# Kernel tuning notes

Hardware: AMD Instinct MI355X
Metric: run time of the kernel (lower is better)

## Reference

```python
import jax, jax.numpy as jnp
import numpy as np
from jax import lax

# dims: S=seq_len, B=batch, D=word dim, HE=encoder hidden, HD=decoder hidden,
# E=atomic embedding dim, A=num_atomic, T=max_steps, SOS=start token id
S, B, D = 48, 64, 300
HE, HD, E, A, T, SOS = 300, 256, 50, 128, 50, 1


def _u(key, shape, scale):
    return jax.random.uniform(key, shape, jnp.float32, -scale, scale)


def setup_inputs() -> dict:
    key = jax.random.key(0)
    ks = iter(jax.random.split(key, 64))
    inp = {"word_vectors": jax.random.normal(next(ks), (S, B, D), jnp.float32)}
    se = 1.0 / np.sqrt(HE)
    for l, din in ((0, D), (1, 2 * HE)):
        for d in ("f", "b"):
            inp[f"e{l}{d}_Wih"] = _u(next(ks), (3 * HE, din), se)
            inp[f"e{l}{d}_Whh"] = _u(next(ks), (3 * HE, HE), se)
            inp[f"e{l}{d}_bih"] = _u(next(ks), (3 * HE,), se)
            inp[f"e{l}{d}_bhh"] = _u(next(ks), (3 * HE,), se)
    sd = 1.0 / np.sqrt(HD)
    for l, din in ((0, E), (1, HD)):
        inp[f"d{l}_Wih"] = _u(next(ks), (3 * HD, din), sd)
        inp[f"d{l}_Whh"] = _u(next(ks), (3 * HD, HD), sd)
        inp[f"d{l}_bih"] = _u(next(ks), (3 * HD,), sd)
        inp[f"d{l}_bhh"] = _u(next(ks), (3 * HD,), sd)
    emb = jax.random.normal(next(ks), (A, E), jnp.float32)
    inp["emb"] = emb.at[0].set(0.0)  # padding_idx=0
    inp["Wout"] = _u(next(ks), (A, HD), sd)
    inp["bout"] = _u(next(ks), (A,), sd)
    so = 1.0 / np.sqrt(D)
    inp["Wh0"] = _u(next(ks), (2 * HD, D), so)
    inp["bh0"] = _u(next(ks), (2 * HD,), so)
    return inp


def gru_cell(x, h, Wih, Whh, bih, bhh):
    # PyTorch GRU cell semantics
    gi = x @ Wih.T + bih
    gh = h @ Whh.T + bhh
    ir, iz, inn = jnp.split(gi, 3, axis=-1)
    hr, hz, hn = jnp.split(gh, 3, axis=-1)
    r = jax.nn.sigmoid(ir + hr)
    z = jax.nn.sigmoid(iz + hz)
    n = jnp.tanh(inn + r * hn)
    return (1.0 - z) * n + z * h


def gru_layer(xs, Wih, Whh, bih, bhh, reverse=False):
    # xs: [S, B, din] -> [S, B, H]; h0 = zeros (torch default)
    h0 = jnp.zeros((xs.shape[1], Whh.shape[1]), xs.dtype)
    def step(h, x):
        hn = gru_cell(x, h, Wih, Whh, bih, bhh)
        return hn, hn
    _, ys = lax.scan(step, h0, xs, reverse=reverse)
    return ys


def reference(word_vectors, e0f_Wih, e0f_Whh, e0f_bih, e0f_bhh, e0b_Wih, e0b_Whh, e0b_bih, e0b_bhh, e1f_Wih, e1f_Whh, e1f_bih, e1f_bhh, e1b_Wih, e1b_Whh, e1b_bih, e1b_bhh, d0_Wih, d0_Whh, d0_bih, d0_bhh, d1_Wih, d1_Whh, d1_bih, d1_bhh, emb, Wout, bout, Wh0, bh0):
    # --- encoder: 2-layer bidirectional GRU (eval mode: no dropout) ---
    x0f = gru_layer(word_vectors, e0f_Wih, e0f_Whh, e0f_bih, e0f_bhh, reverse=False)
    x0b = gru_layer(word_vectors, e0b_Wih, e0b_Whh, e0b_bih, e0b_bhh, reverse=True)
    x0 = jnp.concatenate([x0f, x0b], axis=-1)  # [S,B,2*HE]
    x1f = gru_layer(x0, e1f_Wih, e1f_Whh, e1f_bih, e1f_bhh, reverse=False)
    x1b = gru_layer(x0, e1b_Wih, e1b_Whh, e1b_bih, e1b_bhh, reverse=True)
    enc = x1f + x1b  # view(S,B,2,HE).sum(dim=2) of concat == sum of directions

    N = S * B
    h = jnp.tanh(enc @ Wh0.T + bh0).reshape(N, 2, HD)  # [N,2,HD]
    h0, h1 = h[:, 0], h[:, 1]
    e = jnp.broadcast_to(emb[SOS], (N, E))

    def step(carry, _):
        h0, h1, e = carry
        h0n = gru_cell(e, h0, d0_Wih, d0_Whh, d0_bih, d0_bhh)
        h1n = gru_cell(h0n, h1, d1_Wih, d1_Whh, d1_bih, d1_bhh)
        y = jax.nn.log_softmax(h1n @ Wout.T + bout, axis=-1)  # [N,A]
        p = jnp.argmax(y, axis=-1)
        return (h0n, h1n, emb[p]), y

    _, Y = lax.scan(step, (h0, h1, e), None, length=T)  # [T,N,A]
    return Y.reshape(T, S, B, A)[:-1]
```

## Files before the change

### kernel.cpp

```cpp
#include <hip/hip_runtime.h>
#include <math.h>

#define S_ 48
#define B_ 64
#define D_ 300
#define HE_ 300
#define HD_ 256
#define E_ 50
#define A_ 128
#define T_ 50
#define N_ (S_*B_)
#define NR 6

__device__ __forceinline__ float sigm(float x){ return 1.0f/(1.0f + expf(-x)); }

template<int MODE>
__global__ __launch_bounds__(256)
void gemm_bias_kernel(const float* __restrict__ A, const float* __restrict__ W,
                      const float* __restrict__ bias, float* __restrict__ C,
                      float* __restrict__ C2, int M, int N, int K)
{
  __shared__ float As[16][64];
  __shared__ float Ws[16][64];
  const int tid = threadIdx.x;
  const int bm = blockIdx.y * 64;
  const int bn = blockIdx.x * 64;
  const int tx = tid & 15, ty = tid >> 4;
  const int lr = tid >> 2;
  const int lk = (tid & 3) << 2;
  float acc[4][4] = {{0.f}};
  for (int kb = 0; kb < K; kb += 16) {
    {
      const int row = bm + lr;
      const int k = kb + lk;
      const float* ap = A + (size_t)row * K + k;
      float4 v = make_float4(0.f,0.f,0.f,0.f);
      if (k + 3 < K) v = *reinterpret_cast<const float4*>(ap);
      else {
        if (k   < K) v.x = ap[0];
        if (k+1 < K) v.y = ap[1];
        if (k+2 < K) v.z = ap[2];
        if (k+3 < K) v.w = ap[3];
      }
      As[lk][lr]=v.x; As[lk+1][lr]=v.y; As[lk+2][lr]=v.z; As[lk+3][lr]=v.w;
    }
    {
      const int col = bn + lr;
      const int k = kb + lk;
      float4 v = make_float4(0.f,0.f,0.f,0.f);
      if (col < N) {
        const float* wp = W + (size_t)col * K + k;
        if (k + 3 < K) v = *reinterpret_cast<const float4*>(wp);
        else {
          if (k   < K) v.x = wp[0];
          if (k+1 < K) v.y = wp[1];
          if (k+2 < K) v.z = wp[2];
          if (k+3 < K) v.w = wp[3];
        }
      }
      Ws[lk][lr]=v.x; Ws[lk+1][lr]=v.y; Ws[lk+2][lr]=v.z; Ws[lk+3][lr]=v.w;
    }
    __syncthreads();
    #pragma unroll
    for (int kk = 0; kk < 16; ++kk) {
      float4 a4 = *reinterpret_cast<const float4*>(&As[kk][ty<<2]);
      float4 w4 = *reinterpret_cast<const float4*>(&Ws[kk][tx<<2]);
      const float* a = reinterpret_cast<const float*>(&a4);
      const float* w = reinterpret_cast<const float*>(&w4);
      #pragma unroll
      for (int i = 0; i < 4; ++i)
        #pragma unroll
        for (int j = 0; j < 4; ++j)
          acc[i][j] = fmaf(a[i], w[j], acc[i][j]);
    }
    __syncthreads();
  }
  #pragma unroll
  for (int i = 0; i < 4; ++i) {
    const int m = bm + (ty<<2) + i;
    #pragma unroll
    for (int j = 0; j < 4; ++j) {
      const int n = bn + (tx<<2) + j;
      if (n < N) {
        float v = acc[i][j] + bias[n];
        if (MODE == 0) {
          C[(size_t)m*N + n] = v;
        } else {
          v = tanhf(v);
          if (n < HD_) C[(size_t)m*HD_ + n] = v;
          else         C2[(size_t)m*HD_ + (n-HD_)] = v;
        }
      }
    }
  }
}

__device__ __forceinline__ void tile_mac(const float (*As)[64], const float (*Ws)[16][36],
                                         int tcol, int trow,
                                         float* accr, float* accz, float* accn)
{
  #pragma unroll
  for (int kk = 0; kk < 32; kk += 4) {
    float4 wr4 = *reinterpret_cast<const float4*>(&Ws[0][tcol][kk]);
    float4 wz4 = *reinterpret_cast<const float4*>(&Ws[1][tcol][kk]);
    float4 wn4 = *reinterpret_cast<const float4*>(&Ws[2][tcol][kk]);
    const float* wr = reinterpret_cast<const float*>(&wr4);
    const float* wz = reinterpret_cast<const float*>(&wz4);
    const float* wn = reinterpret_cast<const float*>(&wn4);
    #pragma unroll
    for (int u = 0; u < 4; ++u) {
      float4 a4 = *reinterpret_cast<const float4*>(&As[kk+u][trow]);
      const float* a = reinterpret_cast<const float*>(&a4);
      #pragma unroll
      for (int q = 0; q < 4; ++q) {
        accr[q] = fmaf(a[q], wr[u], accr[q]);
        accz[q] = fmaf(a[q], wz[u], accz[q]);
        accn[q] = fmaf(a[q], wn[u], accn[q]);
      }
    }
  }
}

__global__ __launch_bounds__(256)
void enc_step_kernel(const float* __restrict__ gi_f, const float* __restrict__ gi_b,
                     const float* __restrict__ Whh_f, const float* __restrict__ Whh_b,
                     const float* __restrict__ bhh_f, const float* __restrict__ bhh_b,
                     const float* __restrict__ hin_f, float* __restrict__ hout_f,
                     const float* __restrict__ hin_b, float* __restrict__ hout_b,
                     float* __restrict__ out, int t, int layer)
{
  const int dir = blockIdx.z;
  const float* gi  = dir ? gi_b  : gi_f;
  const float* W   = dir ? Whh_b : Whh_f;
  const float* bhh = dir ? bhh_b : bhh_f;
  const float* hin = dir ? hin_b : hin_f;
  float* hout = dir ? hout_b : hout_f;
  const int tt = dir ? (S_-1 - t) : t;

  __shared__ float As[32][64];
  __shared__ float Ws[3][16][36];
  const int tid = threadIdx.x;
  const int bn = blockIdx.x * 16;
  const int tcol = tid & 15;
  const int trow = (tid >> 4) << 2;
  float accr[4]={0,0,0,0}, accz[4]={0,0,0,0}, accn[4]={0,0,0,0};

  for (int kb = 0; kb < HE_; kb += 32) {
    __syncthreads();
    #pragma unroll
    for (int j = 0; j < 2; ++j) {
      int i = tid + j*256;
      int row = i >> 3;
      int k = (i & 7) << 2;
      const float* ap = hin + (size_t)row*HE_ + kb + k;
      float4 v = make_float4(0.f,0.f,0.f,0.f);
      if (kb + k + 3 < HE_) v = *reinterpret_cast<const float4*>(ap);
      else {
        if (kb+k   < HE_) v.x = ap[0];
        if (kb+k+1 < HE_) v.y = ap[1];
        if (kb+k+2 < HE_) v.z = ap[2];
        if (kb+k+3 < HE_) v.w = ap[3];
      }
      As[k  ][row] = v.x; As[k+1][row] = v.y; As[k+2][row] = v.z; As[k+3][row] = v.w;
    }
    #pragma unroll
    for (int j = 0; j < 6; ++j) {
      int i = tid + j*256;
      int g = i >> 9;
      int c = (i >> 5) & 15;
      int k = i & 31;
      float v = 0.0f;
      if (bn + c < HE_ && kb + k < HE_) v = W[(size_t)(g*HE_ + bn + c)*HE_ + kb + k];
      Ws[g][c][k] = v;
    }
    __syncthreads();
    tile_mac(As, Ws, tcol, trow, accr, accz, accn);
  }

  const int jcol = bn + tcol;
  if (jcol < HE_) {
    #pragma unroll
    for (int i = 0; i < 4; ++i) {
      const int row = trow + i;
      const size_t gbase = (size_t)(tt*B_ + row) * (3*HE_);
      float gr = gi[gbase + jcol];
      float gz = gi[gbase + HE_ + jcol];
      float gn = gi[gbase + 2*HE_ + jcol];
      float r = sigm(gr + accr[i] + bhh[jcol]);
      float z = sigm(gz + accz[i] + bhh[HE_ + jcol]);
      float n = tanhf(gn + r*(accn[i] + bhh[2*HE_ + jcol]));
      float ho = hin[(size_t)row*HE_ + jcol];
      float hn = (1.0f - z)*n + z*ho;
      hout[(size_t)row*HE_ + jcol] = hn;
      if (layer == 0) out[(size_t)(tt*B_ + row)*(2*HE_) + dir*HE_ + jcol] = hn;
      else            out[(size_t)(tt*B_ + row)*HE_ + jcol] += hn;
    }
  }
}

__global__ __launch_bounds__(256)
void transpose_kernel(const float* __restrict__ in, float* __restrict__ out,
                      int NC, int NK)
{
  int idx = blockIdx.x * 256 + threadIdx.x;
  if (idx < NC*NK) {
    int cI = idx / NK, kI = idx % NK;
    out[(size_t)kI*NC + cI] = in[idx];
  }
}

__global__ __launch_bounds__(512, 2)
void dec_persistent(const float* __restrict__ WihT0,
                    const float* __restrict__ WhhT0,
                    const float* __restrict__ WihT1,
                    const float* __restrict__ WhhT1,
                    const float* __restrict__ WoutT,
                    const float* __restrict__ bih0, const float* __restrict__ bhh0,
                    const float* __restrict__ bih1, const float* __restrict__ bhh1,
                    const float* __restrict__ bout,
                    const float* __restrict__ emb,
                    const float* __restrict__ h0init, const float* __restrict__ h1init,
                    float* __restrict__ Y)
{
  __shared__ float h0s[12][256];
  __shared__ float h1s[12][256];
  __shared__ float es[12][52];
  const int tid = threadIdx.x;
  const int bb = blockIdx.x;
  const int R0 = bb * 12;
  const int c  = tid & 255;
  const int half = tid >> 8;
  const int r0 = half * NR;

  for (int i = tid; i < 12*64; i += 512) {
    int r = i >> 6;
    int k = (i & 63) << 2;
    *reinterpret_cast<float4*>(&h0s[r][k]) =
        *reinterpret_cast<const float4*>(&h0init[(size_t)(R0+r)*HD_ + k]);
    *reinterpret_cast<float4*>(&h1s[r][k]) =
        *reinterpret_cast<const float4*>(&h1init[(size_t)(R0+r)*HD_ + k]);
  }
  for (int i = tid; i < 12*E_; i += 512) {
    int r = i / E_, k = i % E_;
    es[r][k] = emb[E_ + k];
  }
  const float b0r = bih0[c] + bhh0[c];
  const float b0z = bih0[HD_+c] + bhh0[HD_+c];
  const float b0ni = bih0[2*HD_+c];
  const float b0nh = bhh0[2*HD_+c];
  const float b1r = bih1[c] + bhh1[c];
  const float b1z = bih1[HD_+c] + bhh1[HD_+c];
  const float b1ni = bih1[2*HD_+c];
  const float b1nh = bhh1[2*HD_+c];
  const float bo0 = bout[tid & 63];
  const float bo1 = bout[64 + (tid & 63)];
  __syncthreads();

  for (int s = 0; s < T_-1; ++s) {
    float ar[NR], az[NR], ani[NR], anh[NR];
    #pragma unroll
    for (int r = 0; r < NR; ++r) { ar[r]=0.f; az[r]=0.f; ani[r]=0.f; anh[r]=0.f; }
    for (int k = 0; k < E_; k += 2) {
      const float* wk = WihT0 + (size_t)k*768;
      float wr0=wk[c],     wz0=wk[HD_+c],     wn0=wk[2*HD_+c];
      float wr1=wk[768+c], wz1=wk[768+HD_+c], wn1=wk[768+2*HD_+c];
      #pragma unroll
      for (int r = 0; r < NR; ++r) {
        float2 x = *reinterpret_cast<const float2*>(&es[r0+r][k]);
        ar[r]=fmaf(x.x,wr0,ar[r]);  ar[r]=fmaf(x.y,wr1,ar[r]);
        az[r]=fmaf(x.x,wz0,az[r]);  az[r]=fmaf(x.y,wz1,az[r]);
        ani[r]=fmaf(x.x,wn0,ani[r]); ani[r]=fmaf(x.y,wn1,ani[r]);
      }
    }
    for (int k = 0; k < HD_; k += 4) {
      float wr[4], wz[4], wn[4];
      #pragma unroll
      for (int u = 0; u < 4; ++u) {
        const float* wk = WhhT0 + (size_t)(k+u)*768;
        wr[u]=wk[c]; wz[u]=wk[HD_+c]; wn[u]=wk[2*HD_+c];
      }
      #pragma unroll
      for (int r = 0; r < NR; ++r) {
        float4 x = *reinterpret_cast<const float4*>(&h0s[r0+r][k]);
        ar[r]=fmaf(x.x,wr[0],ar[r]); ar[r]=fmaf(x.y,wr[1],ar[r]);
        ar[r]=fmaf(x.z,wr[2],ar[r]); ar[r]=fmaf(x.w,wr[3],ar[r]);
        az[r]=fmaf(x.x,wz[0],az[r]); az[r]=fmaf(x.y,wz[1],az[r]);
        az[r]=fmaf(x.z,wz[2],az[r]); az[r]=fmaf(x.w,wz[3],az[r]);
        anh[r]=fmaf(x.x,wn[0],anh[r]); anh[r]=fmaf(x.y,wn[1],anh[r]);
        anh[r]=fmaf(x.z,wn[2],anh[r]); anh[r]=fmaf(x.w,wn[3],anh[r]);
      }
    }
    __syncthreads();
    {
      float hnew[NR];
      #pragma unroll
      for (int r = 0; r < NR; ++r) {
        float rg = sigm(ar[r] + b0r);
        float zg = sigm(az[r] + b0z);
        float ng = tanhf(ani[r] + b0ni + rg*(anh[r] + b0nh));
        float hold = h0s[r0+r][c];
        hnew[r] = (1.0f - zg)*ng + zg*hold;
      }
      #pragma unroll
      for (int r = 0; r < NR; ++r) h0s[r0+r][c] = hnew[r];
    }
    __syncthreads();
    #pragma unroll
    for (int r = 0; r < NR; ++r) { ar[r]=0.f; az[r]=0.f; ani[r]=0.f; anh[r]=0.f; }
    for (int k = 0; k < HD_; k += 4) {
      float wr[4], wz[4], wn[4];
      #pragma unroll
      for (int u = 0; u < 4; ++u) {
        const float* wk = WihT1 + (size_t)(k+u)*768;
        wr[u]=wk[c]; wz[u]=wk[HD_+c]; wn[u]=wk[2*HD_+c];
      }
      #pragma unroll
      for (int r = 0; r < NR; ++r) {
        float4 x = *reinterpret_cast<const float4*>(&h0s[r0+r][k]);
        ar[r]=fmaf(x.x,wr[0],ar[r]); ar[r]=fmaf(x.y,wr[1],ar[r]);
        ar[r]=fmaf(x.z,wr[2],ar[r]); ar[r]=fmaf(x.w,wr[3],ar[r]);
        az[r]=fmaf(x.x,wz[0],az[r]); az[r]=fmaf(x.y,wz[1],az[r]);
        az[r]=fmaf(x.z,wz[2],az[r]); az[r]=fmaf(x.w,wz[3],az[r]);
        ani[r]=fmaf(x.x,wn[0],ani[r]); ani[r]=fmaf(x.y,wn[1],ani[r]);
        ani[r]=fmaf(x.z,wn[2],ani[r]); ani[r]=fmaf(x.w,wn[3],ani[r]);
      }
    }
    for (int k = 0; k < HD_; k += 4) {
      float wr[4], wz[4], wn[4];
      #pragma unroll
      for (int u = 0; u < 4; ++u) {
        const float* wk = WhhT1 + (size_t)(k+u)*768;
        wr[u]=wk[c]; wz[u]=wk[HD_+c]; wn[u]=wk[2*HD_+c];
      }
      #pragma unroll
      for (int r = 0; r < NR; ++r) {
        float4 x = *reinterpret_cast<const float4*>(&h1s[r0+r][k]);
        ar[r]=fmaf(x.x,wr[0],ar[r]); ar[r]=fmaf(x.y,wr[1],ar[r]);
        ar[r]=fmaf(x.z,wr[2],ar[r]); ar[r]=fmaf(x.w,wr[3],ar[r]);
        az[r]=fmaf(x.x,wz[0],az[r]); az[r]=fmaf(x.y,wz[1],az[r]);
        az[r]=fmaf(x.z,wz[2],az[r]); az[r]=fmaf(x.w,wz[3],az[r]);
        anh[r]=fmaf(x.x,wn[0],anh[r]); anh[r]=fmaf(x.y,wn[1],anh[r]);
        anh[r]=fmaf(x.z,wn[2],anh[r]); anh[r]=fmaf(x.w,wn[3],anh[r]);
      }
    }
    __syncthreads();
    {
      float hnew[NR];
      #pragma unroll
      for (int r = 0; r < NR; ++r) {
        float rg = sigm(ar[r] + b1r);
        float zg = sigm(az[r] + b1z);
        float ng = tanhf(ani[r] + b1ni + rg*(anh[r] + b1nh));
        float hold = h1s[r0+r][c];
        hnew[r] = (1.0f - zg)*ng + zg*hold;
      }
      #pragma unroll
      for (int r = 0; r < NR; ++r) h1s[r0+r][c] = hnew[r];
    }
    __syncthreads();
    {
      const int w = tid >> 6;
      const int lane = tid & 63;
      if (w < 6) {
        const int row0 = 2*w;
        float a00=0.f, a01=0.f, a10=0.f, a11=0.f;
        for (int k = 0; k < HD_; k += 2) {
          float w00 = WoutT[(size_t)k*A_ + lane];
          float w01 = WoutT[(size_t)k*A_ + 64 + lane];
          float w10 = WoutT[(size_t)(k+1)*A_ + lane];
          float w11 = WoutT[(size_t)(k+1)*A_ + 64 + lane];
          float2 hv0 = *reinterpret_cast<const float2*>(&h1s[row0][k]);
          float2 hv1 = *reinterpret_cast<const float2*>(&h1s[row0+1][k]);
          a00 = fmaf(hv0.x, w00, a00); a00 = fmaf(hv0.y, w10, a00);
          a01 = fmaf(hv0.x, w01, a01); a01 = fmaf(hv0.y, w11, a01);
          a10 = fmaf(hv1.x, w00, a10); a10 = fmaf(hv1.y, w10, a10);
          a11 = fmaf(hv1.x, w01, a11); a11 = fmaf(hv1.y, w11, a11);
        }
        float va[2][2] = {{a00,a01},{a10,a11}};
        #pragma unroll
        for (int rr = 0; rr < 2; ++rr) {
          const int row = row0 + rr;
          float v0 = va[rr][0] + bo0;
          float v1 = va[rr][1] + bo1;
          float mx = fmaxf(v0, v1);
          #pragma unroll
          for (int off = 32; off >= 1; off >>= 1) mx = fmaxf(mx, __shfl_xor(mx, off));
          float sum = expf(v0 - mx) + expf(v1 - mx);
          #pragma unroll
          for (int off = 32; off >= 1; off >>= 1) sum += __shfl_xor(sum, off);
          float lz = mx + logf(sum);
          float* Yr = Y + ((size_t)s*N_ + R0 + row)*A_;
          Yr[lane]      = v0 - lz;
          Yr[64 + lane] = v1 - lz;
          float bv; int bi;
          if (v0 >= v1) { bv = v0; bi = lane; } else { bv = v1; bi = 64 + lane; }
          #pragma unroll
          for (int off = 32; off >= 1; off >>= 1) {
            float ov = __shfl_xor(bv, off);
            int   oi = __shfl_xor(bi, off);
            if (ov > bv || (ov == bv && oi < bi)) { bv = ov; bi = oi; }
          }
          if (lane < E_) es[row][lane] = emb[(size_t)bi*E_ + lane];
        }
      }
    }
    __syncthreads();
  }
}

extern "C" void kernel_launch(void* const* d_in, const int* in_sizes, int n_in,
                              void* d_out, int out_size, void* d_ws, size_t ws_size,
                              hipStream_t stream)
{
  (void)in_sizes; (void)n_in; (void)out_size; (void)ws_size;
  const float* wv      = (const float*)d_in[0];
  const float* e0f_Wih = (const float*)d_in[1];
  const float* e0f_Whh = (const float*)d_in[2];
  const float* e0f_bih = (const float*)d_in[3];
  const float* e0f_bhh = (const float*)d_in[4];
  const float* e0b_Wih = (const float*)d_in[5];
  const float* e0b_Whh = (const float*)d_in[6];
  const float* e0b_bih = (const float*)d_in[7];
  const float* e0b_bhh = (const float*)d_in[8];
  const float* e1f_Wih = (const float*)d_in[9];
  const float* e1f_Whh = (const float*)d_in[10];
  const float* e1f_bih = (const float*)d_in[11];
  const float* e1f_bhh = (const float*)d_in[12];
  const float* e1b_Wih = (const float*)d_in[13];
  const float* e1b_Whh = (const float*)d_in[14];
  const float* e1b_bih = (const float*)d_in[15];
  const float* e1b_bhh = (const float*)d_in[16];
  const float* d0_Wih  = (const float*)d_in[17];
  const float* d0_Whh  = (const float*)d_in[18];
  const float* d0_bih  = (const float*)d_in[19];
  const float* d0_bhh  = (const float*)d_in[20];
  const float* d1_Wih  = (const float*)d_in[21];
  const float* d1_Whh  = (const float*)d_in[22];
  const float* d1_bih  = (const float*)d_in[23];
  const float* d1_bhh  = (const float*)d_in[24];
  const float* emb     = (const float*)d_in[25];
  const float* Wout    = (const float*)d_in[26];
  const float* bout    = (const float*)d_in[27];
  const float* Wh0     = (const float*)d_in[28];
  const float* bh0     = (const float*)d_in[29];

  float* ws = (float*)d_ws;
  size_t off = 0;
  auto alloc = [&](size_t n){ float* q = ws + off; off += n; return q; };
  float* giA = alloc((size_t)N_*3*HE_);
  float* giB = alloc((size_t)N_*3*HE_);
  float* x0  = alloc((size_t)N_*2*HE_);
  float* enc = alloc((size_t)N_*HE_);
  float* hfA = alloc((size_t)B_*HE_);
  float* hfB = alloc((size_t)B_*HE_);
  float* hbA = alloc((size_t)B_*HE_);
  float* hbB = alloc((size_t)B_*HE_);
  float* h0A = giA;
  float* h1A = giA + (size_t)N_*HD_;
  float* WihT0 = x0;
  float* WhhT0 = WihT0 + (size_t)E_*768;
  float* WihT1 = WhhT0 + (size_t)HD_*768;
  float* WhhT1 = WihT1 + (size_t)HD_*768;
  float* WoutT = WhhT1 + (size_t)HD_*768;
  float* Y = (float*)d_out;

  const dim3 blk(256);

  gemm_bias_kernel<0><<<dim3(15,48), blk, 0, stream>>>(wv, e0f_Wih, e0f_bih, giA, nullptr, N_, 3*HE_, D_);
  gemm_bias_kernel<0><<<dim3(15,48), blk, 0, stream>>>(wv, e0b_Wih, e0b_bih, giB, nullptr, N_, 3*HE_, D_);
  hipMemsetAsync(hfA, 0, (size_t)B_*HE_*sizeof(float), stream);
  hipMemsetAsync(hbA, 0, (size_t)B_*HE_*sizeof(float), stream);
  {
    float* hfi = hfA; float* hfo = hfB; float* hbi = hbA; float* hbo = hbB;
    for (int t = 0; t < S_; ++t) {
      enc_step_kernel<<<dim3(19,1,2), blk, 0, stream>>>(giA, giB, e0f_Whh, e0b_Whh,
          e0f_bhh, e0b_bhh, hfi, hfo, hbi, hbo, x0, t, 0);
      float* tmp = hfi; hfi = hfo; hfo = tmp;
      tmp = hbi; hbi = hbo; hbo = tmp;
    }
  }
  gemm_bias_kernel<0><<<dim3(15,48), blk, 0, stream>>>(x0, e1f_Wih, e1f_bih, giA, nullptr, N_, 3*HE_, 2*HE_);
  gemm_bias_kernel<0><<<dim3(15,48), blk, 0, stream>>>(x0, e1b_Wih, e1b_bih, giB, nullptr, N_, 3*HE_, 2*HE_);
  hipMemsetAsync(hfA, 0, (size_t)B_*HE_*sizeof(float), stream);
  hipMemsetAsync(hbA, 0, (size_t)B_*HE_*sizeof(float), stream);
  hipMemsetAsync(enc, 0, (size_t)N_*HE_*sizeof(float), stream);
  {
    float* hfi = hfA; float* hfo = hfB; float* hbi = hbA; float* hbo = hbB;
    for (int t = 0; t < S_; ++t) {
      enc_step_kernel<<<dim3(19,1,2), blk, 0, stream>>>(giA, giB, e1f_Whh, e1b_Whh,
          e1f_bhh, e1b_bhh, hfi, hfo, hbi, hbo, enc, t, 1);
      float* tmp = hfi; hfi = hfo; hfo = tmp;
      tmp = hbi; hbi = hbo; hbo = tmp;
    }
  }
  gemm_bias_kernel<1><<<dim3(8,48), blk, 0, stream>>>(enc, Wh0, bh0, h0A, h1A, N_, 2*HD_, HE_);
  transpose_kernel<<<dim3(150), blk, 0, stream>>>(d0_Wih, WihT0, 3*HD_, E_);
  transpose_kernel<<<dim3(768), blk, 0, stream>>>(d0_Whh, WhhT0, 3*HD_, HD_);
  transpose_kernel<<<dim3(768), blk, 0, stream>>>(d1_Wih, WihT1, 3*HD_, HD_);
  transpose_kernel<<<dim3(768), blk, 0, stream>>>(d1_Whh, WhhT1, 3*HD_, HD_);
  transpose_kernel<<<dim3(128), blk, 0, stream>>>(Wout,   WoutT, A_,    HD_);
  dec_persistent<<<dim3(N_/12), dim3(512), 0, stream>>>(
      WihT0, WhhT0, WihT1, WhhT1, WoutT,
      d0_bih, d0_bhh, d1_bih, d1_bhh, bout,
      emb, h0A, h1A, Y);
}
```

Before: 6.856 ms.

## Split encoder rows across blocks and widen decoder with float4-packed weights

The encoder step kernel now splits the 64 batch rows over four blocks in y, with one row per thread. This quadruples the number of blocks per recurrent step for better CU coverage, at the cost of reloading the Whh tile in each row block. The decoder persistent kernel grows from 512 to 1024 threads, so each thread handles 3 rows instead of 6. It also reads weights from a k4-major float4-packed layout, so each weight load is one 16-byte access, and the weight packing now runs earlier, before the layer-1 encoder loop. The risk is register pressure or spills from the aggressive launch bounds on 1024-thread blocks.

```diff
diff --git a/kernel.cpp b/kernel.cpp
--- a/kernel.cpp
+++ b/kernel.cpp
@@ -10,7 +10,6 @@
 #define A_ 128
 #define T_ 50
 #define N_ (S_*B_)
-#define NR 6
 
 __device__ __forceinline__ float sigm(float x){ return 1.0f/(1.0f + expf(-x)); }
 
@@ -95,32 +94,6 @@
   }
 }
 
-__device__ __forceinline__ void tile_mac(const float (*As)[64], const float (*Ws)[16][36],
-                                         int tcol, int trow,
-                                         float* accr, float* accz, float* accn)
-{
-  #pragma unroll
-  for (int kk = 0; kk < 32; kk += 4) {
-    float4 wr4 = *reinterpret_cast<const float4*>(&Ws[0][tcol][kk]);
-    float4 wz4 = *reinterpret_cast<const float4*>(&Ws[1][tcol][kk]);
-    float4 wn4 = *reinterpret_cast<const float4*>(&Ws[2][tcol][kk]);
-    const float* wr = reinterpret_cast<const float*>(&wr4);
-    const float* wz = reinterpret_cast<const float*>(&wz4);
-    const float* wn = reinterpret_cast<const float*>(&wn4);
-    #pragma unroll
-    for (int u = 0; u < 4; ++u) {
-      float4 a4 = *reinterpret_cast<const float4*>(&As[kk+u][trow]);
-      const float* a = reinterpret_cast<const float*>(&a4);
-      #pragma unroll
-      for (int q = 0; q < 4; ++q) {
-        accr[q] = fmaf(a[q], wr[u], accr[q]);
-        accz[q] = fmaf(a[q], wz[u], accz[q]);
-        accn[q] = fmaf(a[q], wn[u], accn[q]);
-      }
-    }
-  }
-}
-
 __global__ __launch_bounds__(256)
 void enc_step_kernel(const float* __restrict__ gi_f, const float* __restrict__ gi_b,
                      const float* __restrict__ Whh_f, const float* __restrict__ Whh_b,
@@ -137,22 +110,21 @@
   float* hout = dir ? hout_b : hout_f;
   const int tt = dir ? (S_-1 - t) : t;
 
-  __shared__ float As[32][64];
+  __shared__ float As[32][17];
   __shared__ float Ws[3][16][36];
   const int tid = threadIdx.x;
   const int bn = blockIdx.x * 16;
+  const int rb = blockIdx.y * 16;
   const int tcol = tid & 15;
-  const int trow = (tid >> 4) << 2;
-  float accr[4]={0,0,0,0}, accz[4]={0,0,0,0}, accn[4]={0,0,0,0};
+  const int trow = tid >> 4;
+  float accr=0.f, accz=0.f, accn=0.f;
 
   for (int kb = 0; kb < HE_; kb += 32) {
     __syncthreads();
-    #pragma unroll
-    for (int j = 0; j < 2; ++j) {
-      int i = tid + j*256;
-      int row = i >> 3;
-      int k = (i & 7) << 2;
-      const float* ap = hin + (size_t)row*HE_ + kb + k;
+    if (tid < 128) {
+      int row = tid >> 3;
+      int k = (tid & 7) << 2;
+      const float* ap = hin + (size_t)(rb+row)*HE_ + kb + k;
       float4 v = make_float4(0.f,0.f,0.f,0.f);
       if (kb + k + 3 < HE_) v = *reinterpret_cast<const float4*>(ap);
       else {
@@ -161,60 +133,77 @@
         if (kb+k+2 < HE_) v.z = ap[2];
         if (kb+k+3 < HE_) v.w = ap[3];
       }
-      As[k  ][row] = v.x; As[k+1][row] = v.y; As[k+2][row] = v.z; As[k+3][row] = v.w;
+      As[k][row]=v.x; As[k+1][row]=v.y; As[k+2][row]=v.z; As[k+3][row]=v.w;
     }
     #pragma unroll
     for (int j = 0; j < 6; ++j) {
       int i = tid + j*256;
       int g = i >> 9;
-      int c = (i >> 5) & 15;
+      int cc = (i >> 5) & 15;
       int k = i & 31;
       float v = 0.0f;
-      if (bn + c < HE_ && kb + k < HE_) v = W[(size_t)(g*HE_ + bn + c)*HE_ + kb + k];
-      Ws[g][c][k] = v;
-    }
-    __syncthreads();
-    tile_mac(As, Ws, tcol, trow, accr, accz, accn);
-  }
-
+      if (bn + cc < HE_ && kb + k < HE_) v = W[(size_t)(g*HE_ + bn + cc)*HE_ + kb + k];
+      Ws[g][cc][k] = v;
+    }
+    __syncthreads();
+    #pragma unroll
+    for (int kk = 0; kk < 32; kk += 4) {
+      float4 wr4 = *reinterpret_cast<const float4*>(&Ws[0][tcol][kk]);
+      float4 wz4 = *reinterpret_cast<const float4*>(&Ws[1][tcol][kk]);
+      float4 wn4 = *reinterpret_cast<const float4*>(&Ws[2][tcol][kk]);
+      const float* wr = reinterpret_cast<const float*>(&wr4);
+      const float* wz = reinterpret_cast<const float*>(&wz4);
+      const float* wn = reinterpret_cast<const float*>(&wn4);
+      #pragma unroll
+      for (int u = 0; u < 4; ++u) {
+        float a = As[kk+u][trow];
+        accr = fmaf(a, wr[u], accr);
+        accz = fmaf(a, wz[u], accz);
+        accn = fmaf(a, wn[u], accn);
+      }
+    }
+  }
   const int jcol = bn + tcol;
+  const int row = rb + trow;
   if (jcol < HE_) {
-    #pragma unroll
-    for (int i = 0; i < 4; ++i) {
-      const int row = trow + i;
-      const size_t gbase = (size_t)(tt*B_ + row) * (3*HE_);
-      float gr = gi[gbase + jcol];
-      float gz = gi[gbase + HE_ + jcol];
-      float gn = gi[gbase + 2*HE_ + jcol];
-      float r = sigm(gr + accr[i] + bhh[jcol]);
-      float z = sigm(gz + accz[i] + bhh[HE_ + jcol]);
-      float n = tanhf(gn + r*(accn[i] + bhh[2*HE_ + jcol]));
-      float ho = hin[(size_t)row*HE_ + jcol];
-      float hn = (1.0f - z)*n + z*ho;
-      hout[(size_t)row*HE_ + jcol] = hn;
-      if (layer == 0) out[(size_t)(tt*B_ + row)*(2*HE_) + dir*HE_ + jcol] = hn;
-      else            out[(size_t)(tt*B_ + row)*HE_ + jcol] += hn;
-    }
+    const size_t gbase = (size_t)(tt*B_ + row) * (3*HE_);
+    float gr = gi[gbase + jcol];
+    float gz = gi[gbase + HE_ + jcol];
+    float gn = gi[gbase + 2*HE_ + jcol];
+    float r = sigm(gr + accr + bhh[jcol]);
+    float z = sigm(gz + accz + bhh[HE_ + jcol]);
+    float n = tanhf(gn + r*(accn + bhh[2*HE_ + jcol]));
+    float ho = hin[(size_t)row*HE_ + jcol];
+    float hn = (1.0f - z)*n + z*ho;
+    hout[(size_t)row*HE_ + jcol] = hn;
+    if (layer == 0) out[(size_t)(tt*B_ + row)*(2*HE_) + dir*HE_ + jcol] = hn;
+    else            out[(size_t)(tt*B_ + row)*HE_ + jcol] += hn;
   }
 }
 
 __global__ __launch_bounds__(256)
-void transpose_kernel(const float* __restrict__ in, float* __restrict__ out,
-                      int NC, int NK)
+void pack4_kernel(const float* __restrict__ W, float4* __restrict__ P,
+                  int NC, int NK, int K4)
 {
   int idx = blockIdx.x * 256 + threadIdx.x;
-  if (idx < NC*NK) {
-    int cI = idx / NK, kI = idx % NK;
-    out[(size_t)kI*NC + cI] = in[idx];
-  }
+  if (idx >= NC * K4) return;
+  int k4 = idx / NC, gc = idx % NC;
+  int k = k4 << 2;
+  const float* wp = W + (size_t)gc * NK + k;
+  float4 v = make_float4(0.f,0.f,0.f,0.f);
+  if (k   < NK) v.x = wp[0];
+  if (k+1 < NK) v.y = wp[1];
+  if (k+2 < NK) v.z = wp[2];
+  if (k+3 < NK) v.w = wp[3];
+  P[(size_t)k4 * NC + gc] = v;
 }
 
-__global__ __launch_bounds__(512, 2)
-void dec_persistent(const float* __restrict__ WihT0,
-                    const float* __restrict__ WhhT0,
-                    const float* __restrict__ WihT1,
-                    const float* __restrict__ WhhT1,
-                    const float* __restrict__ WoutT,
+__global__ __launch_bounds__(1024, 4)
+void dec_persistent(const float4* __restrict__ Wih0P,
+                    const float4* __restrict__ Whh0P,
+                    const float4* __restrict__ Wih1P,
+                    const float4* __restrict__ Whh1P,
+                    const float4* __restrict__ WoP,
                     const float* __restrict__ bih0, const float* __restrict__ bhh0,
                     const float* __restrict__ bih1, const float* __restrict__ bhh1,
                     const float* __restrict__ bout,
@@ -226,23 +215,22 @@
   __shared__ float h1s[12][256];
   __shared__ float es[12][52];
   const int tid = threadIdx.x;
-  const int bb = blockIdx.x;
-  const int R0 = bb * 12;
-  const int c  = tid & 255;
-  const int half = tid >> 8;
-  const int r0 = half * NR;
-
-  for (int i = tid; i < 12*64; i += 512) {
-    int r = i >> 6;
-    int k = (i & 63) << 2;
+  const int R0 = blockIdx.x * 12;
+  const int c = tid & 255;
+  const int q = tid >> 8;
+  const int r0 = q * 3;
+  const int lane = tid & 63;
+
+  for (int i = tid; i < 12*64; i += 1024) {
+    int r = i >> 6, k = (i & 63) << 2;
     *reinterpret_cast<float4*>(&h0s[r][k]) =
         *reinterpret_cast<const float4*>(&h0init[(size_t)(R0+r)*HD_ + k]);
     *reinterpret_cast<float4*>(&h1s[r][k]) =
         *reinterpret_cast<const float4*>(&h1init[(size_t)(R0+r)*HD_ + k]);
   }
-  for (int i = tid; i < 12*E_; i += 512) {
-    int r = i / E_, k = i % E_;
-    es[r][k] = emb[E_ + k];
+  for (int i = tid; i < 12*52; i += 1024) {
+    int r = i / 52, k = i % 52;
+    es[r][k] = (k < E_) ? emb[E_ + k] : 0.0f;
   }
   const float b0r = bih0[c] + bhh0[c];
   const float b0z = bih0[HD_+c] + bhh0[HD_+c];
@@ -252,49 +240,47 @@
   const float b1z = bih1[HD_+c] + bhh1[HD_+c];
   const float b1ni = bih1[2*HD_+c];
   const float b1nh = bhh1[2*HD_+c];
-  const float bo0 = bout[tid & 63];
-  const float bo1 = bout[64 + (tid & 63)];
+  const float bo0 = bout[lane];
+  const float bo1 = bout[64 + lane];
   __syncthreads();
 
   for (int s = 0; s < T_-1; ++s) {
-    float ar[NR], az[NR], ani[NR], anh[NR];
-    #pragma unroll
-    for (int r = 0; r < NR; ++r) { ar[r]=0.f; az[r]=0.f; ani[r]=0.f; anh[r]=0.f; }
-    for (int k = 0; k < E_; k += 2) {
-      const float* wk = WihT0 + (size_t)k*768;
-      float wr0=wk[c],     wz0=wk[HD_+c],     wn0=wk[2*HD_+c];
-      float wr1=wk[768+c], wz1=wk[768+HD_+c], wn1=wk[768+2*HD_+c];
-      #pragma unroll
-      for (int r = 0; r < NR; ++r) {
-        float2 x = *reinterpret_cast<const float2*>(&es[r0+r][k]);
-        ar[r]=fmaf(x.x,wr0,ar[r]);  ar[r]=fmaf(x.y,wr1,ar[r]);
-        az[r]=fmaf(x.x,wz0,az[r]);  az[r]=fmaf(x.y,wz1,az[r]);
-        ani[r]=fmaf(x.x,wn0,ani[r]); ani[r]=fmaf(x.y,wn1,ani[r]);
-      }
-    }
-    for (int k = 0; k < HD_; k += 4) {
-      float wr[4], wz[4], wn[4];
-      #pragma unroll
-      for (int u = 0; u < 4; ++u) {
-        const float* wk = WhhT0 + (size_t)(k+u)*768;
-        wr[u]=wk[c]; wz[u]=wk[HD_+c]; wn[u]=wk[2*HD_+c];
-      }
-      #pragma unroll
-      for (int r = 0; r < NR; ++r) {
-        float4 x = *reinterpret_cast<const float4*>(&h0s[r0+r][k]);
-        ar[r]=fmaf(x.x,wr[0],ar[r]); ar[r]=fmaf(x.y,wr[1],ar[r]);
-        ar[r]=fmaf(x.z,wr[2],ar[r]); ar[r]=fmaf(x.w,wr[3],ar[r]);
-        az[r]=fmaf(x.x,wz[0],az[r]); az[r]=fmaf(x.y,wz[1],az[r]);
-        az[r]=fmaf(x.z,wz[2],az[r]); az[r]=fmaf(x.w,wz[3],az[r]);
-        anh[r]=fmaf(x.x,wn[0],anh[r]); anh[r]=fmaf(x.y,wn[1],anh[r]);
-        anh[r]=fmaf(x.z,wn[2],anh[r]); anh[r]=fmaf(x.w,wn[3],anh[r]);
+    float ar[3]={0,0,0}, az[3]={0,0,0}, ani[3]={0,0,0}, anh[3]={0,0,0};
+    for (int k4 = 0; k4 < 13; ++k4) {
+      float4 wr = Wih0P[k4*768 + c];
+      float4 wz = Wih0P[k4*768 + 256 + c];
+      float4 wn = Wih0P[k4*768 + 512 + c];
+      #pragma unroll
+      for (int r = 0; r < 3; ++r) {
+        float4 x = *reinterpret_cast<const float4*>(&es[r0+r][k4<<2]);
+        ar[r]=fmaf(x.x,wr.x,ar[r]); ar[r]=fmaf(x.y,wr.y,ar[r]);
+        ar[r]=fmaf(x.z,wr.z,ar[r]); ar[r]=fmaf(x.w,wr.w,ar[r]);
+        az[r]=fmaf(x.x,wz.x,az[r]); az[r]=fmaf(x.y,wz.y,az[r]);
+        az[r]=fmaf(x.z,wz.z,az[r]); az[r]=fmaf(x.w,wz.w,az[r]);
+        ani[r]=fmaf(x.x,wn.x,ani[r]); ani[r]=fmaf(x.y,wn.y,ani[r]);
+        ani[r]=fmaf(x.z,wn.z,ani[r]); ani[r]=fmaf(x.w,wn.w,ani[r]);
+      }
+    }
+    for (int k4 = 0; k4 < 64; ++k4) {
+      float4 wr = Whh0P[k4*768 + c];
+      float4 wz = Whh0P[k4*768 + 256 + c];
+      float4 wn = Whh0P[k4*768 + 512 + c];
+      #pragma unroll
+      for (int r = 0; r < 3; ++r) {
+        float4 x = *reinterpret_cast<const float4*>(&h0s[r0+r][k4<<2]);
+        ar[r]=fmaf(x.x,wr.x,ar[r]); ar[r]=fmaf(x.y,wr.y,ar[r]);
+        ar[r]=fmaf(x.z,wr.z,ar[r]); ar[r]=fmaf(x.w,wr.w,ar[r]);
+        az[r]=fmaf(x.x,wz.x,az[r]); az[r]=fmaf(x.y,wz.y,az[r]);
+        az[r]=fmaf(x.z,wz.z,az[r]); az[r]=fmaf(x.w,wz.w,az[r]);
+        anh[r]=fmaf(x.x,wn.x,anh[r]); anh[r]=fmaf(x.y,wn.y,anh[r]);
+        anh[r]=fmaf(x.z,wn.z,anh[r]); anh[r]=fmaf(x.w,wn.w,anh[r]);
       }
     }
     __syncthreads();
     {
-      float hnew[NR];
-      #pragma unroll
-      for (int r = 0; r < NR; ++r) {
+      float hnew[3];
+      #pragma unroll
+      for (int r = 0; r < 3; ++r) {
         float rg = sigm(ar[r] + b0r);
         float zg = sigm(az[r] + b0z);
         float ng = tanhf(ani[r] + b0ni + rg*(anh[r] + b0nh));
@@ -302,52 +288,46 @@
         hnew[r] = (1.0f - zg)*ng + zg*hold;
       }
       #pragma unroll
-      for (int r = 0; r < NR; ++r) h0s[r0+r][c] = hnew[r];
+      for (int r = 0; r < 3; ++r) h0s[r0+r][c] = hnew[r];
     }
     __syncthreads();
     #pragma unroll
-    for (int r = 0; r < NR; ++r) { ar[r]=0.f; az[r]=0.f; ani[r]=0.f; anh[r]=0.f; }
-    for (int k = 0; k < HD_; k += 4) {
-      float wr[4], wz[4], wn[4];
-      #pragma unroll
-      for (int u = 0; u < 4; ++u) {
-        const float* wk = WihT1 + (size_t)(k+u)*768;
-        wr[u]=wk[c]; wz[u]=wk[HD_+c]; wn[u]=wk[2*HD_+c];
-      }
-      #pragma unroll
-      for (int r = 0; r < NR; ++r) {
-        float4 x = *reinterpret_cast<const float4*>(&h0s[r0+r][k]);
-        ar[r]=fmaf(x.x,wr[0],ar[r]); ar[r]=fmaf(x.y,wr[1],ar[r]);
-        ar[r]=fmaf(x.z,wr[2],ar[r]); ar[r]=fmaf(x.w,wr[3],ar[r]);
-        az[r]=fmaf(x.x,wz[0],az[r]); az[r]=fmaf(x.y,wz[1],az[r]);
-        az[r]=fmaf(x.z,wz[2],az[r]); az[r]=fmaf(x.w,wz[3],az[r]);
-        ani[r]=fmaf(x.x,wn[0],ani[r]); ani[r]=fmaf(x.y,wn[1],ani[r]);
-        ani[r]=fmaf(x.z,wn[2],ani[r]); ani[r]=fmaf(x.w,wn[3],ani[r]);
-      }
-    }
-    for (int k = 0; k < HD_; k += 4) {
-      float wr[4], wz[4], wn[4];
-      #pragma unroll
-      for (int u = 0; u < 4; ++u) {
-        const float* wk = WhhT1 + (size_t)(k+u)*768;
-        wr[u]=wk[c]; wz[u]=wk[HD_+c]; wn[u]=wk[2*HD_+c];
-      }
-      #pragma unroll
-      for (int r = 0; r < NR; ++r) {
-        float4 x = *reinterpret_cast<const float4*>(&h1s[r0+r][k]);
-        ar[r]=fmaf(x.x,wr[0],ar[r]); ar[r]=fmaf(x.y,wr[1],ar[r]);
-        ar[r]=fmaf(x.z,wr[2],ar[r]); ar[r]=fmaf(x.w,wr[3],ar[r]);
-        az[r]=fmaf(x.x,wz[0],az[r]); az[r]=fmaf(x.y,wz[1],az[r]);
-        az[r]=fmaf(x.z,wz[2],az[r]); az[r]=fmaf(x.w,wz[3],az[r]);
-        anh[r]=fmaf(x.x,wn[0],anh[r]); anh[r]=fmaf(x.y,wn[1],anh[r]);
-        anh[r]=fmaf(x.z,wn[2],anh[r]); anh[r]=fmaf(x.w,wn[3],anh[r]);
+    for (int r = 0; r < 3; ++r) { ar[r]=0.f; az[r]=0.f; ani[r]=0.f; anh[r]=0.f; }
+    for (int k4 = 0; k4 < 64; ++k4) {
+      float4 wr = Wih1P[k4*768 + c];
+      float4 wz = Wih1P[k4*768 + 256 + c];
+      float4 wn = Wih1P[k4*768 + 512 + c];
+      #pragma unroll
+      for (int r = 0; r < 3; ++r) {
+        float4 x = *reinterpret_cast<const float4*>(&h0s[r0+r][k4<<2]);
+        ar[r]=fmaf(x.x,wr.x,ar[r]); ar[r]=fmaf(x.y,wr.y,ar[r]);
+        ar[r]=fmaf(x.z,wr.z,ar[r]); ar[r]=fmaf(x.w,wr.w,ar[r]);
+        az[r]=fmaf(x.x,wz.x,az[r]); az[r]=fmaf(x.y,wz.y,az[r]);
+        az[r]=fmaf(x.z,wz.z,az[r]); az[r]=fmaf(x.w,wz.w,az[r]);
+        ani[r]=fmaf(x.x,wn.x,ani[r]); ani[r]=fmaf(x.y,wn.y,ani[r]);
+        ani[r]=fmaf(x.z,wn.z,ani[r]); ani[r]=fmaf(x.w,wn.w,ani[r]);
+      }
+    }
+    for (int k4 = 0; k4 < 64; ++k4) {
+      float4 wr = Whh1P[k4*768 + c];
+      float4 wz = Whh1P[k4*768 + 256 + c];
+      float4 wn = Whh1P[k4*768 + 512 + c];
+      #pragma unroll
+      for (int r = 0; r < 3; ++r) {
+        float4 x = *reinterpret_cast<const float4*>(&h1s[r0+r][k4<<2]);
+        ar[r]=fmaf(x.x,wr.x,ar[r]); ar[r]=fmaf(x.y,wr.y,ar[r]);
+        ar[r]=fmaf(x.z,wr.z,ar[r]); ar[r]=fmaf(x.w,wr.w,ar[r]);
+        az[r]=fmaf(x.x,wz.x,az[r]); az[r]=fmaf(x.y,wz.y,az[r]);
+        az[r]=fmaf(x.z,wz.z,az[r]); az[r]=fmaf(x.w,wz.w,az[r]);
+        anh[r]=fmaf(x.x,wn.x,anh[r]); anh[r]=fmaf(x.y,wn.y,anh[r]);
+        anh[r]=fmaf(x.z,wn.z,anh[r]); anh[r]=fmaf(x.w,wn.w,anh[r]);
       }
     }
     __syncthreads();
     {
-      float hnew[NR];
-      #pragma unroll
-      for (int r = 0; r < NR; ++r) {
+      float hnew[3];
+      #pragma unroll
+      for (int r = 0; r < 3; ++r) {
         float rg = sigm(ar[r] + b1r);
         float zg = sigm(az[r] + b1z);
         float ng = tanhf(ani[r] + b1ni + rg*(anh[r] + b1nh));
@@ -355,53 +335,44 @@
         hnew[r] = (1.0f - zg)*ng + zg*hold;
       }
       #pragma unroll
-      for (int r = 0; r < NR; ++r) h1s[r0+r][c] = hnew[r];
+      for (int r = 0; r < 3; ++r) h1s[r0+r][c] = hnew[r];
     }
     __syncthreads();
     {
       const int w = tid >> 6;
-      const int lane = tid & 63;
-      if (w < 6) {
-        const int row0 = 2*w;
-        float a00=0.f, a01=0.f, a10=0.f, a11=0.f;
-        for (int k = 0; k < HD_; k += 2) {
-          float w00 = WoutT[(size_t)k*A_ + lane];
-          float w01 = WoutT[(size_t)k*A_ + 64 + lane];
-          float w10 = WoutT[(size_t)(k+1)*A_ + lane];
-          float w11 = WoutT[(size_t)(k+1)*A_ + 64 + lane];
-          float2 hv0 = *reinterpret_cast<const float2*>(&h1s[row0][k]);
-          float2 hv1 = *reinterpret_cast<const float2*>(&h1s[row0+1][k]);
-          a00 = fmaf(hv0.x, w00, a00); a00 = fmaf(hv0.y, w10, a00);
-          a01 = fmaf(hv0.x, w01, a01); a01 = fmaf(hv0.y, w11, a01);
-          a10 = fmaf(hv1.x, w00, a10); a10 = fmaf(hv1.y, w10, a10);
-          a11 = fmaf(hv1.x, w01, a11); a11 = fmaf(hv1.y, w11, a11);
+      if (w < 12) {
+        const int row = w;
+        float a0 = 0.f, a1 = 0.f;
+        for (int k4 = 0; k4 < 64; ++k4) {
+          float4 w0 = WoP[k4*128 + lane];
+          float4 w1 = WoP[k4*128 + 64 + lane];
+          float4 h = *reinterpret_cast<const float4*>(&h1s[row][k4<<2]);
+          a0 = fmaf(h.x,w0.x,a0); a0 = fmaf(h.y,w0.y,a0);
+          a0 = fmaf(h.z,w0.z,a0); a0 = fmaf(h.w,w0.w,a0);
+          a1 = fmaf(h.x,w1.x,a1); a1 = fmaf(h.y,w1.y,a1);
+          a1 = fmaf(h.z,w1.z,a1); a1 = fmaf(h.w,w1.w,a1);
         }
-        float va[2][2] = {{a00,a01},{a10,a11}};
+        float v0 = a0 + bo0;
+        float v1 = a1 + bo1;
+        float mx = fmaxf(v0, v1);
         #pragma unroll
-        for (int rr = 0; rr < 2; ++rr) {
-          const int row = row0 + rr;
-          float v0 = va[rr][0] + bo0;
-          float v1 = va[rr][1] + bo1;
-          float mx = fmaxf(v0, v1);
-          #pragma unroll
-          for (int off = 32; off >= 1; off >>= 1) mx = fmaxf(mx, __shfl_xor(mx, off));
-          float sum = expf(v0 - mx) + expf(v1 - mx);
-          #pragma unroll
-          for (int off = 32; off >= 1; off >>= 1) sum += __shfl_xor(sum, off);
-          float lz = mx + logf(sum);
-          float* Yr = Y + ((size_t)s*N_ + R0 + row)*A_;
-          Yr[lane]      = v0 - lz;
-          Yr[64 + lane] = v1 - lz;
-          float bv; int bi;
-          if (v0 >= v1) { bv = v0; bi = lane; } else { bv = v1; bi = 64 + lane; }
-          #pragma unroll
-          for (int off = 32; off >= 1; off >>= 1) {
-            float ov = __shfl_xor(bv, off);
-            int   oi = __shfl_xor(bi, off);
-            if (ov > bv || (ov == bv && oi < bi)) { bv = ov; bi = oi; }
-          }
-          if (lane < E_) es[row][lane] = emb[(size_t)bi*E_ + lane];
+        for (int off = 32; off >= 1; off >>= 1) mx = fmaxf(mx, __shfl_xor(mx, off));
+        float sum = expf(v0 - mx) + expf(v1 - mx);
+        #pragma unroll
+        for (int off = 32; off >= 1; off >>= 1) sum += __shfl_xor(sum, off);
+        float lz = mx + logf(sum);
+        float* Yr = Y + ((size_t)s*N_ + R0 + row)*A_;
+        Yr[lane]      = v0 - lz;
+        Yr[64 + lane] = v1 - lz;
+        float bv; int bi;
+        if (v0 >= v1) { bv = v0; bi = lane; } else { bv = v1; bi = 64 + lane; }
+        #pragma unroll
+        for (int off = 32; off >= 1; off >>= 1) {
+          float ov = __shfl_xor(bv, off);
+          int   oi = __shfl_xor(bi, off);
+          if (ov > bv || (ov == bv && oi < bi)) { bv = ov; bi = oi; }
         }
+        if (lane < E_) es[row][lane] = emb[(size_t)bi*E_ + lane];
       }
     }
     __syncthreads();
@@ -457,11 +428,11 @@
   float* hbB = alloc((size_t)B_*HE_);
   float* h0A = giA;
   float* h1A = giA + (size_t)N_*HD_;
-  float* WihT0 = x0;
-  float* WhhT0 = WihT0 + (size_t)E_*768;
-  float* WihT1 = WhhT0 + (size_t)HD_*768;
-  float* WhhT1 = WihT1 + (size_t)HD_*768;
-  float* WoutT = WhhT1 + (size_t)HD_*768;
+  float4* Wih0P = (float4*)x0;
+  float4* Whh0P = Wih0P + (size_t)13*768;
+  float4* Wih1P = Whh0P + (size_t)64*768;
+  float4* Whh1P = Wih1P + (size_t)64*768;
+  float4* WoP   = Whh1P + (size_t)64*768;
   float* Y = (float*)d_out;
 
   const dim3 blk(256);
@@ -473,7 +444,7 @@
   {
     float* hfi = hfA; float* hfo = hfB; float* hbi = hbA; float* hbo = hbB;
     for (int t = 0; t < S_; ++t) {
-      enc_step_kernel<<<dim3(19,1,2), blk, 0, stream>>>(giA, giB, e0f_Whh, e0b_Whh,
+      enc_step_kernel<<<dim3(19,4,2), blk, 0, stream>>>(giA, giB, e0f_Whh, e0b_Whh,
           e0f_bhh, e0b_bhh, hfi, hfo, hbi, hbo, x0, t, 0);
       float* tmp = hfi; hfi = hfo; hfo = tmp;
       tmp = hbi; hbi = hbo; hbo = tmp;
@@ -481,26 +452,26 @@
   }
   gemm_bias_kernel<0><<<dim3(15,48), blk, 0, stream>>>(x0, e1f_Wih, e1f_bih, giA, nullptr, N_, 3*HE_, 2*HE_);
   gemm_bias_kernel<0><<<dim3(15,48), blk, 0, stream>>>(x0, e1b_Wih, e1b_bih, giB, nullptr, N_, 3*HE_, 2*HE_);
+  pack4_kernel<<<dim3(39),  blk, 0, stream>>>(d0_Wih, Wih0P, 3*HD_, E_,  13);
+  pack4_kernel<<<dim3(192), blk, 0, stream>>>(d0_Whh, Whh0P, 3*HD_, HD_, 64);
+  pack4_kernel<<<dim3(192), blk, 0, stream>>>(d1_Wih, Wih1P, 3*HD_, HD_, 64);
+  pack4_kernel<<<dim3(192), blk, 0, stream>>>(d1_Whh, Whh1P, 3*HD_, HD_, 64);
+  pack4_kernel<<<dim3(32),  blk, 0, stream>>>(Wout,   WoP,   A_,    HD_, 64);
   hipMemsetAsync(hfA, 0, (size_t)B_*HE_*sizeof(float), stream);
   hipMemsetAsync(hbA, 0, (size_t)B_*HE_*sizeof(float), stream);
   hipMemsetAsync(enc, 0, (size_t)N_*HE_*sizeof(float), stream);
   {
     float* hfi = hfA; float* hfo = hfB; float* hbi = hbA; float* hbo = hbB;
     for (int t = 0; t < S_; ++t) {
-      enc_step_kernel<<<dim3(19,1,2), blk, 0, stream>>>(giA, giB, e1f_Whh, e1b_Whh,
+      enc_step_kernel<<<dim3(19,4,2), blk, 0, stream>>>(giA, giB, e1f_Whh, e1b_Whh,
           e1f_bhh, e1b_bhh, hfi, hfo, hbi, hbo, enc, t, 1);
       float* tmp = hfi; hfi = hfo; hfo = tmp;
       tmp = hbi; hbi = hbo; hbo = tmp;
     }
   }
   gemm_bias_kernel<1><<<dim3(8,48), blk, 0, stream>>>(enc, Wh0, bh0, h0A, h1A, N_, 2*HD_, HE_);
-  transpose_kernel<<<dim3(150), blk, 0, stream>>>(d0_Wih, WihT0, 3*HD_, E_);
-  transpose_kernel<<<dim3(768), blk, 0, stream>>>(d0_Whh, WhhT0, 3*HD_, HD_);
-  transpose_kernel<<<dim3(768), blk, 0, stream>>>(d1_Wih, WihT1, 3*HD_, HD_);
-  transpose_kernel<<<dim3(768), blk, 0, stream>>>(d1_Whh, WhhT1, 3*HD_, HD_);
-  transpose_kernel<<<dim3(128), blk, 0, stream>>>(Wout,   WoutT, A_,    HD_);
-  dec_persistent<<<dim3(N_/12), dim3(512), 0, stream>>>(
-      WihT0, WhhT0, WihT1, WhhT1, WoutT,
+  dec_persistent<<<dim3(N_/12), dim3(1024), 0, stream>>>(
+      Wih0P, Whh0P, Wih1P, Whh1P, WoP,
       d0_bih, d0_bhh, d1_bih, d1_bhh, bout,
       emb, h0A, h1A, Y);
 }
```

Measured after the change: 15.43 ms. 125% more time.
